# Performance work log

Hardware: AMD Instinct MI355X
Metric: run time of the kernel (lower is better)

## Reference

```python
import jax, jax.numpy as jnp
import numpy as np

NF, NA, H, L, R, B = 100000, 4000, 256, 4, 4, 3
E_FA, E_AF, E_FF, E_AA = 200000, 200000, 400000, 40000
N = NF + NA


def setup_inputs() -> dict:
    key = jax.random.key(0)
    ks = jax.random.split(key, 18)
    inp = {}
    inp["x_flight"] = jax.random.normal(ks[0], (NF, 32), jnp.float32)
    inp["x_airport"] = jax.random.normal(ks[1], (NA, 16), jnp.float32)
    # per-node-type encoder Linears (stored as [in, H] so y = x @ W + b)
    inp["enc_w_flight"] = jax.random.normal(ks[2], (32, H), jnp.float32) / np.sqrt(32.0).astype(np.float32)
    inp["enc_b_flight"] = jnp.zeros((H,), jnp.float32)
    inp["enc_w_airport"] = jax.random.normal(ks[3], (16, H), jnp.float32) / np.sqrt(16.0).astype(np.float32)
    inp["enc_b_airport"] = jnp.zeros((H,), jnp.float32)
    # stacked per-layer RGCNConv params: basis decomposition W_r = sum_b comp[r,b] * basis[b]
    inp["basis"] = jax.random.normal(ks[4], (L, B, H, H), jnp.float32) * 0.02
    inp["comp"] = jax.random.normal(ks[5], (L, R, B), jnp.float32)
    inp["root"] = jax.random.normal(ks[6], (L, H, H), jnp.float32) * 0.02
    inp["conv_bias"] = jnp.zeros((L, H), jnp.float32)
    inp["ln_gamma"] = jnp.ones((L, H), jnp.float32)
    inp["ln_beta"] = jnp.zeros((L, H), jnp.float32)
    inp["ro_w"] = jax.random.normal(ks[7], (H, 1), jnp.float32) / np.sqrt(float(H)).astype(np.float32)
    inp["ro_b"] = jnp.zeros((1,), jnp.float32)
    # hetero edge indices (row 0 = src local id, row 1 = dst local id)
    inp["ei_fa"] = jnp.stack([jax.random.randint(ks[8], (E_FA,), 0, NF),
                               jax.random.randint(ks[9], (E_FA,), 0, NA)]).astype(jnp.int32)
    inp["ei_af"] = jnp.stack([jax.random.randint(ks[10], (E_AF,), 0, NA),
                               jax.random.randint(ks[11], (E_AF,), 0, NF)]).astype(jnp.int32)
    inp["ei_ff"] = jnp.stack([jax.random.randint(ks[12], (E_FF,), 0, NF),
                               jax.random.randint(ks[13], (E_FF,), 0, NF)]).astype(jnp.int32)
    inp["ei_aa"] = jnp.stack([jax.random.randint(ks[14], (E_AA,), 0, NA),
                               jax.random.randint(ks[15], (E_AA,), 0, NA)]).astype(jnp.int32)
    return inp


def _layernorm(x, g, b, eps=1e-5):
    mu = jnp.mean(x, axis=-1, keepdims=True)
    var = jnp.mean(jnp.square(x - mu), axis=-1, keepdims=True)
    return (x - mu) * jax.lax.rsqrt(var + eps) * g + b


def _build_graph(ei_fa, ei_af, ei_ff, ei_aa):
    # node offsets: flight=0, airport=NF (node_types order = ['flight','airport'])
    src = jnp.concatenate([ei_fa[0], ei_af[0] + NF, ei_ff[0], ei_aa[0] + NF])
    dst = jnp.concatenate([ei_fa[1] + NF, ei_af[1], ei_ff[1], ei_aa[1] + NF])
    et = jnp.concatenate([jnp.full((E_FA,), 0, jnp.int32), jnp.full((E_AF,), 1, jnp.int32),
                          jnp.full((E_FF,), 2, jnp.int32), jnp.full((E_AA,), 3, jnp.int32)])
    return src, dst, et


def reference(x_flight, x_airport, enc_w_flight, enc_b_flight, enc_w_airport, enc_b_airport,
              basis, comp, root, conv_bias, ln_gamma, ln_beta, ro_w, ro_b,
              ei_fa, ei_af, ei_ff, ei_aa):
    hf = x_flight @ enc_w_flight + enc_b_flight    # [NF, H]
    ha = x_airport @ enc_w_airport + enc_b_airport  # [NA, H]
    x = jnp.concatenate([hf, ha], axis=0)           # [N, H]

    src, dst, et = _build_graph(ei_fa, ei_af, ei_ff, ei_aa)
    seg = et * N + dst                              # composite (relation, target-node) segment id
    cnt = jax.ops.segment_sum(jnp.ones(src.shape, x.dtype), seg, num_segments=R * N)
    denom = jnp.maximum(cnt.reshape(R, N, 1), 1.0)  # per-relation in-degree (mean aggr)

    for l in range(L):
        x_res = x
        W = jnp.einsum('rb,bio->rio', comp[l], basis[l])                 # [R, H, H]
        agg = jax.ops.segment_sum(x[src], seg, num_segments=R * N)
        agg = agg.reshape(R, N, H) / denom                                # per-relation mean of x_j
        h = jnp.einsum('rnh,rho->no', agg, W) + x @ root[l] + conv_bias[l]
        h = _layernorm(h, ln_gamma[l], ln_beta[l])
        h = jnp.where(h > 0, h, 0.1 * h)                                  # leaky_relu(0.1)
        x = h + x_res                                                     # dropout is identity in eval

    return (x[:NF] @ ro_w + ro_b)[:, 0]             # readout over flight nodes, squeeze(-1)
```

## Files before the change

kernel.cpp:

```cpp
#include <hip/hip_runtime.h>
#include <cstdint>


namespace {

constexpr int kNF = 100000;
constexpr int kNA = 4000;
constexpr int kN  = 104000;
constexpr int kH  = 256;
constexpr int kL  = 4;
constexpr int kB  = 3;
constexpr int kEFA = 200000;
constexpr int kEAF = 200000;
constexpr int kEFF = 400000;
constexpr int kEAA = 40000;
constexpr int kETOT = 840000;
constexpr int kK = 768;
constexpr int kKA = 512;
constexpr int kSEG = 2 * kNA + 2 * kNF;
constexpr int kScanBlocks = (kSEG + 1023) / 1024;

typedef __attribute__((ext_vector_type(8))) short short8v;
typedef __attribute__((ext_vector_type(4))) float float4v;

__device__ __forceinline__ float b2f(unsigned short u) {
  union { unsigned int i; float f; } v;
  v.i = ((unsigned int)u) << 16;
  return v.f;
}
__device__ __forceinline__ unsigned short f2b(float f) {
  union { float f; unsigned int i; } v;
  v.f = f;
  unsigned int x = v.i;
  x += 0x7fffu + ((x >> 16) & 1u);
  return (unsigned short)(x >> 16);
}

__device__ __forceinline__ void gload16(const unsigned short* gsrc,
                                        unsigned short* lds) {
  __builtin_amdgcn_global_load_lds(
      (const __attribute__((address_space(1))) unsigned int*)gsrc,
      (__attribute__((address_space(3))) unsigned int*)lds, 16, 0, 0);
}

__global__ void k_build_encWt(const float* __restrict__ wf,
                              const float* __restrict__ wa,
                              unsigned short* __restrict__ WtF,
                              unsigned short* __restrict__ WtA) {
  const int idx = blockIdx.x * 256 + threadIdx.x;
  if (idx >= 2 * kH * 32) return;
  const int t = idx / (kH * 32);
  const int rem = idx % (kH * 32);
  const int n = rem >> 5;
  const int k = rem & 31;
  if (t == 0) {
    WtF[n * 32 + k] = f2b(wf[k * kH + n]);
  } else {
    WtA[n * 32 + k] = (k < 16) ? f2b(wa[k * kH + n]) : (unsigned short)0;
  }
}

template <int KIN>
__global__ __launch_bounds__(256) void k_enc_mfma(
    const float* __restrict__ xin, const unsigned short* __restrict__ Wt,
    const float* __restrict__ bias, unsigned short* __restrict__ xout, int M,
    int rowoff) {
  __shared__ __align__(16) unsigned short As[64][40];
  const int tid = threadIdx.x;
  const int wave = tid >> 6;
  const int lane = tid & 63;
  const int fr = lane & 15;
  const int fq = lane >> 4;
  const int ncol0 = wave * 64;
  const int brow = blockIdx.x * 64;

  const int row = tid >> 2;
  const int col0 = (tid & 3) * 8;
  float4 f0 = make_float4(0.f, 0.f, 0.f, 0.f);
  float4 f1 = make_float4(0.f, 0.f, 0.f, 0.f);
  if (brow + row < M) {
    if (col0 < KIN) f0 = *(const float4*)&xin[(size_t)(brow + row) * KIN + col0];
    if (col0 + 4 < KIN)
      f1 = *(const float4*)&xin[(size_t)(brow + row) * KIN + col0 + 4];
  }
  uint4 packed;
  packed.x = (unsigned int)f2b(f0.x) | ((unsigned int)f2b(f0.y) << 16);
  packed.y = (unsigned int)f2b(f0.z) | ((unsigned int)f2b(f0.w) << 16);
  packed.z = (unsigned int)f2b(f1.x) | ((unsigned int)f2b(f1.y) << 16);
  packed.w = (unsigned int)f2b(f1.z) | ((unsigned int)f2b(f1.w) << 16);
  *(uint4*)&As[row][col0] = packed;
  __syncthreads();

  short8v bfrag[4];
#pragma unroll
  for (int ni = 0; ni < 4; ++ni)
    bfrag[ni] = *(const short8v*)&Wt[(size_t)(ncol0 + ni * 16 + fr) * 32 + fq * 8];

  float4v acc[4][4];
#pragma unroll
  for (int mi = 0; mi < 4; ++mi) {
    const short8v afrag = *(const short8v*)&As[mi * 16 + fr][fq * 8];
#pragma unroll
    for (int ni = 0; ni < 4; ++ni)
      acc[mi][ni] = __builtin_amdgcn_mfma_f32_16x16x32_bf16(
          afrag, bfrag[ni], (float4v)(0.f), 0, 0, 0);
  }

#pragma unroll
  for (int ni = 0; ni < 4; ++ni) {
    const int col = ncol0 + ni * 16 + fr;
    const float bb = bias[col];
#pragma unroll
    for (int mi = 0; mi < 4; ++mi) {
      const int row0 = brow + mi * 16 + fq * 4;
#pragma unroll
      for (int reg = 0; reg < 4; ++reg) {
        const int r = row0 + reg;
        if (r < M) xout[(size_t)(rowoff + r) * kH + col] = f2b(acc[mi][ni][reg] + bb);
      }
    }
  }
}

__device__ __forceinline__ void edge_decode(int i, const int* ei_fa,
                                            const int* ei_af, const int* ei_ff,
                                            const int* ei_aa, int& src,
                                            int& dstseg) {
  if (i < kEFA) {
    src = ei_fa[i];
    dstseg = 0 + ei_fa[kEFA + i];
  } else if (i < kEFA + kEAF) {
    const int j = i - kEFA;
    src = kNF + ei_af[j];
    dstseg = kNA + ei_af[kEAF + j];
  } else if (i < kEFA + kEAF + kEFF) {
    const int j = i - kEFA - kEAF;
    src = ei_ff[j];
    dstseg = kNA + kNF + ei_ff[kEFF + j];
  } else {
    const int j = i - kEFA - kEAF - kEFF;
    src = kNF + ei_aa[j];
    dstseg = kNA + 2 * kNF + ei_aa[kEAA + j];
  }
}

__global__ void k_count_all(const int* __restrict__ ei_fa,
                            const int* __restrict__ ei_af,
                            const int* __restrict__ ei_ff,
                            const int* __restrict__ ei_aa,
                            int* __restrict__ cnt) {
  const int i = blockIdx.x * 256 + threadIdx.x;
  if (i >= kETOT) return;
  int src, dstseg;
  edge_decode(i, ei_fa, ei_af, ei_ff, ei_aa, src, dstseg);
  atomicAdd(&cnt[dstseg], 1);
}

__global__ void k_scan1(const int* __restrict__ cnt, int* __restrict__ out,
                        int* __restrict__ bsum, float* __restrict__ invdeg) {
  __shared__ int sh[256];
  const int tid = threadIdx.x;
  const int base = blockIdx.x * 1024 + tid * 4;
  int v[4];
#pragma unroll
  for (int j = 0; j < 4; ++j) v[j] = (base + j < kSEG) ? cnt[base + j] : 0;
#pragma unroll
  for (int j = 0; j < 4; ++j)
    if (base + j < kSEG)
      invdeg[base + j] = 1.0f / (float)(v[j] > 0 ? v[j] : 1);
  const int tsum = v[0] + v[1] + v[2] + v[3];
  sh[tid] = tsum;
  __syncthreads();
  for (int o = 1; o < 256; o <<= 1) {
    int t = (tid >= o) ? sh[tid - o] : 0;
    __syncthreads();
    sh[tid] += t;
    __syncthreads();
  }
  const int excl = sh[tid] - tsum;
  int run = excl;
#pragma unroll
  for (int j = 0; j < 4; ++j) {
    if (base + j < kSEG) out[base + j] = run;
    run += v[j];
  }
  if (tid == 255) bsum[blockIdx.x] = sh[255];
}

__global__ void k_scan2(const int* __restrict__ bsum, int* __restrict__ bpre) {
  __shared__ int sh[256];
  const int tid = threadIdx.x;
  const int v = (tid < kScanBlocks) ? bsum[tid] : 0;
  sh[tid] = v;
  __syncthreads();
  for (int o = 1; o < 256; o <<= 1) {
    int t = (tid >= o) ? sh[tid - o] : 0;
    __syncthreads();
    sh[tid] += t;
    __syncthreads();
  }
  if (tid < kScanBlocks) bpre[tid] = sh[tid] - v;
}

__global__ void k_scan3(int* __restrict__ off, int* __restrict__ cursor,
                        const int* __restrict__ bpre) {
  const int i = blockIdx.x * 256 + threadIdx.x;
  if (i < kSEG) {
    const int val = off[i] + bpre[i >> 10];
    off[i] = val;
    cursor[i] = val;
  }
  if (i == 0) off[kSEG] = kETOT;
}

__global__ void k_fill_all(const int* __restrict__ ei_fa,
                           const int* __restrict__ ei_af,
                           const int* __restrict__ ei_ff,
                           const int* __restrict__ ei_aa,
                           int* __restrict__ cursor, int* __restrict__ elist) {
  const int i = blockIdx.x * 256 + threadIdx.x;
  if (i >= kETOT) return;
  int src, dstseg;
  edge_decode(i, ei_fa, ei_af, ei_ff, ei_aa, src, dstseg);
  const int pos = atomicAdd(&cursor[dstseg], 1);
  elist[pos] = src;
}

__global__ void k_build_Bt(const float* __restrict__ comp_l,
                           const float* __restrict__ basis_l,
                           const float* __restrict__ root_l,
                           unsigned short* __restrict__ BtF,
                           unsigned short* __restrict__ BtA) {
  const int idx = blockIdx.x * 256 + threadIdx.x;
  if (idx >= 2 * kK * kH) return;
  const int t = idx / (kK * kH);
  const int rem = idx % (kK * kH);
  const int n = rem / kK;
  const int k = rem % kK;
  const int slot = k >> 8;
  const int wrow = k & 255;
  float val;
  if (slot == 2) {
    val = root_l[wrow * kH + n];
  } else {
    const int r = (t == 0) ? (slot == 0 ? 1 : 2) : (slot == 0 ? 0 : 3);
    const int io = wrow * kH + n;
    val = comp_l[r * kB + 0] * basis_l[0 * kH * kH + io] +
          comp_l[r * kB + 1] * basis_l[1 * kH * kH + io] +
          comp_l[r * kB + 2] * basis_l[2 * kH * kH + io];
  }
  (t == 0 ? BtF : BtA)[(size_t)n * kK + k] = f2b(val);
}

__global__ __launch_bounds__(256) void k_gather2(
    const unsigned short* __restrict__ x, unsigned short* __restrict__ Aagg,
    const int* __restrict__ off, const int* __restrict__ elist,
    const float* __restrict__ invdeg, int segbase0, int segbase1, int c0,
    int nrows) {
  const int half = threadIdx.x >> 5;
  const int lane = threadIdx.x & 31;
  const int d = blockIdx.x * 8 + half;
  const int slot = blockIdx.y;
  if (d >= nrows) return;
  const int s = (slot == 0 ? segbase0 : segbase1) + c0 + d;
  const int lo = off[s], hi = off[s + 1];
  const float iv = invdeg[s];
  float a0 = 0.f, a1 = 0.f, a2 = 0.f, a3 = 0.f;
  float a4 = 0.f, a5 = 0.f, a6 = 0.f, a7 = 0.f;
  const unsigned short* xl = x + lane * 8;
  int e = lo;
  for (; e + 3 < hi; e += 4) {
    const int s0 = elist[e], s1 = elist[e + 1];
    const int s2 = elist[e + 2], s3 = elist[e + 3];
    const uint4 v0 = *(const uint4*)(xl + (size_t)s0 * kH);
    const uint4 v1 = *(const uint4*)(xl + (size_t)s1 * kH);
    const uint4 v2 = *(const uint4*)(xl + (size_t)s2 * kH);
    const uint4 v3 = *(const uint4*)(xl + (size_t)s3 * kH);
    a0 += b2f((unsigned short)v0.x) + b2f((unsigned short)v1.x) +
          b2f((unsigned short)v2.x) + b2f((unsigned short)v3.x);
    a1 += b2f((unsigned short)(v0.x >> 16)) + b2f((unsigned short)(v1.x >> 16)) +
          b2f((unsigned short)(v2.x >> 16)) + b2f((unsigned short)(v3.x >> 16));
    a2 += b2f((unsigned short)v0.y) + b2f((unsigned short)v1.y) +
          b2f((unsigned short)v2.y) + b2f((unsigned short)v3.y);
    a3 += b2f((unsigned short)(v0.y >> 16)) + b2f((unsigned short)(v1.y >> 16)) +
          b2f((unsigned short)(v2.y >> 16)) + b2f((unsigned short)(v3.y >> 16));
    a4 += b2f((unsigned short)v0.z) + b2f((unsigned short)v1.z) +
          b2f((unsigned short)v2.z) + b2f((unsigned short)v3.z);
    a5 += b2f((unsigned short)(v0.z >> 16)) + b2f((unsigned short)(v1.z >> 16)) +
          b2f((unsigned short)(v2.z >> 16)) + b2f((unsigned short)(v3.z >> 16));
    a6 += b2f((unsigned short)v0.w) + b2f((unsigned short)v1.w) +
          b2f((unsigned short)v2.w) + b2f((unsigned short)v3.w);
    a7 += b2f((unsigned short)(v0.w >> 16)) + b2f((unsigned short)(v1.w >> 16)) +
          b2f((unsigned short)(v2.w >> 16)) + b2f((unsigned short)(v3.w >> 16));
  }
  for (; e < hi; ++e) {
    const int s0 = elist[e];
    const uint4 v0 = *(const uint4*)(xl + (size_t)s0 * kH);
    a0 += b2f((unsigned short)v0.x);
    a1 += b2f((unsigned short)(v0.x >> 16));
    a2 += b2f((unsigned short)v0.y);
    a3 += b2f((unsigned short)(v0.y >> 16));
    a4 += b2f((unsigned short)v0.z);
    a5 += b2f((unsigned short)(v0.z >> 16));
    a6 += b2f((unsigned short)v0.w);
    a7 += b2f((unsigned short)(v0.w >> 16));
  }
  uint4 o;
  o.x = (unsigned int)f2b(a0 * iv) | ((unsigned int)f2b(a1 * iv) << 16);
  o.y = (unsigned int)f2b(a2 * iv) | ((unsigned int)f2b(a3 * iv) << 16);
  o.z = (unsigned int)f2b(a4 * iv) | ((unsigned int)f2b(a5 * iv) << 16);
  o.w = (unsigned int)f2b(a6 * iv) | ((unsigned int)f2b(a7 * iv) << 16);
  *(uint4*)&Aagg[(size_t)d * kKA + slot * kH + lane * 8] = o;
}

__global__ __launch_bounds__(256) void k_gemm_fused(
    const unsigned short* __restrict__ Aagg,
    const unsigned short* __restrict__ xcur, unsigned short* __restrict__ xnxt,
    const unsigned short* __restrict__ Bt, const float* __restrict__ bias,
    const float* __restrict__ gamma, const float* __restrict__ beta, int M,
    int grow0) {
  __shared__ __align__(16) unsigned short As[3][64][32];
  __shared__ __align__(16) unsigned short Bs[3][256][32];
  __shared__ float redS[4][64];
  __shared__ float redQ[4][64];
  __shared__ float stat[64][2];

  const int tid = threadIdx.x;
  const int wave = tid >> 6;
  const int lane = tid & 63;
  const int fr = lane & 15;
  const int fq = lane >> 4;
  const int ncol0 = wave * 64;
  const int brow = blockIdx.x * 64;

  const int srow = lane >> 2;
  const int sg = (lane & 3) ^ (srow & 3);
  const int arow = wave * 16 + srow;
  const unsigned short* Asrc_agg = Aagg + (size_t)(brow + arow) * kKA + sg * 8;
  const unsigned short* Asrc_x =
      xcur + (size_t)(grow0 + brow + arow) * kH + sg * 8;
  const unsigned short* Bsrc = Bt + (size_t)(wave * 64 + srow) * kK + sg * 8;

#define STAGE(buf, t)                                                         \
  do {                                                                        \
    const int kb_ = (t) * 32;                                                 \
    gload16((kb_ < kKA) ? (Asrc_agg + kb_) : (Asrc_x + (kb_ - kKA)),          \
            &As[buf][wave * 16][0]);                                          \
    _Pragma("unroll") for (int j_ = 0; j_ < 4; ++j_)                          \
        gload16(Bsrc + (size_t)(j_ * 16) * kK + kb_,                          \
                &Bs[buf][wave * 64 + j_ * 16][0]);                            \
  } while (0)

  float4v acc[4][4];
#pragma unroll
  for (int mi = 0; mi < 4; ++mi)
#pragma unroll
    for (int ni = 0; ni < 4; ++ni) acc[mi][ni] = (float4v)(0.f);

  const int rg = (fr & 3);

  STAGE(0, 0);
  STAGE(1, 1);
  asm volatile("s_waitcnt vmcnt(5)" ::: "memory");
  asm volatile("s_barrier" ::: "memory");

  for (int t = 0; t < 24; ++t) {
    const int cur = t % 3;
    short8v afrag[4], bfrag[4];
#pragma unroll
    for (int mi = 0; mi < 4; ++mi)
      afrag[mi] = *(const short8v*)&As[cur][mi * 16 + fr][(fq ^ rg) * 8];
#pragma unroll
    for (int ni = 0; ni < 4; ++ni)
      bfrag[ni] =
          *(const short8v*)&Bs[cur][ncol0 + ni * 16 + fr][(fq ^ rg) * 8];
    asm volatile("s_waitcnt lgkmcnt(0)" ::: "memory");
    if (t < 22) STAGE((t + 2) % 3, t + 2);
#pragma unroll
    for (int mi = 0; mi < 4; ++mi)
#pragma unroll
      for (int ni = 0; ni < 4; ++ni)
        acc[mi][ni] = __builtin_amdgcn_mfma_f32_16x16x32_bf16(
            afrag[mi], bfrag[ni], acc[mi][ni], 0, 0, 0);
    if (t < 22) {
      asm volatile("s_waitcnt vmcnt(5)" ::: "memory");
    } else {
      asm volatile("s_waitcnt vmcnt(0)" ::: "memory");
    }
    asm volatile("s_barrier" ::: "memory");
  }
#undef STAGE

  float bb[4], gam[4], bet[4];
#pragma unroll
  for (int ni = 0; ni < 4; ++ni) {
    const int col = ncol0 + ni * 16 + fr;
    bb[ni] = bias[col];
    gam[ni] = gamma[col];
    bet[ni] = beta[col];
  }
#pragma unroll
  for (int mi = 0; mi < 4; ++mi)
#pragma unroll
    for (int ni = 0; ni < 4; ++ni)
#pragma unroll
      for (int reg = 0; reg < 4; ++reg) acc[mi][ni][reg] += bb[ni];

#pragma unroll
  for (int mi = 0; mi < 4; ++mi) {
#pragma unroll
    for (int reg = 0; reg < 4; ++reg) {
      float s = 0.f, q = 0.f;
#pragma unroll
      for (int ni = 0; ni < 4; ++ni) {
        const float v = acc[mi][ni][reg];
        s += v;
        q += v * v;
      }
#pragma unroll
      for (int o = 1; o < 16; o <<= 1) {
        s += __shfl_xor(s, o);
        q += __shfl_xor(q, o);
      }
      if (fr == 0) {
        const int rl = mi * 16 + fq * 4 + reg;
        redS[wave][rl] = s;
        redQ[wave][rl] = q;
      }
    }
  }
  __syncthreads();
  if (tid < 64) {
    const float s = redS[0][tid] + redS[1][tid] + redS[2][tid] + redS[3][tid];
    const float q = redQ[0][tid] + redQ[1][tid] + redQ[2][tid] + redQ[3][tid];
    const float mu = s * (1.f / kH);
    const float var = q * (1.f / kH) - mu * mu;
    stat[tid][0] = mu;
    stat[tid][1] = rsqrtf(var + 1e-5f);
  }
  __syncthreads();

#pragma unroll
  for (int mi = 0; mi < 4; ++mi) {
#pragma unroll
    for (int reg = 0; reg < 4; ++reg) {
      const int rl = mi * 16 + fq * 4 + reg;
      const int r = brow + rl;
      if (r >= M) continue;
      const float mu = stat[rl][0];
      const float rs = stat[rl][1];
      const size_t gr = (size_t)(grow0 + r) * kH;
#pragma unroll
      for (int ni = 0; ni < 4; ++ni) {
        const int col = ncol0 + ni * 16 + fr;
        float t = (acc[mi][ni][reg] - mu) * rs * gam[ni] + bet[ni];
        t = t > 0.f ? t : 0.1f * t;
        const float xo = b2f(xcur[gr + col]);
        xnxt[gr + col] = f2b(xo + t);
      }
    }
  }
}

__global__ __launch_bounds__(256) void k_readout(
    const unsigned short* __restrict__ x, const float* __restrict__ w,
    const float* __restrict__ b, float* __restrict__ out) {
  const int wave = threadIdx.x >> 6;
  const int lane = threadIdx.x & 63;
  const int row = blockIdx.x * 4 + wave;
  if (row >= kNF) return;
  const ushort4 v = *(const ushort4*)&x[(size_t)row * kH + (lane << 2)];
  const float4 wv = *(const float4*)&w[lane << 2];
  float s = b2f(v.x) * wv.x + b2f(v.y) * wv.y + b2f(v.z) * wv.z +
            b2f(v.w) * wv.w;
#pragma unroll
  for (int o = 1; o < 64; o <<= 1) s += __shfl_xor(s, o);
  if (lane == 0) out[row] = s + b[0];
}

}

extern "C" void kernel_launch(void* const* d_in, const int* in_sizes, int n_in,
                              void* d_out, int out_size, void* d_ws,
                              size_t ws_size, hipStream_t stream) {
  const float* x_flight = (const float*)d_in[0];
  const float* x_airport = (const float*)d_in[1];
  const float* enc_w_f = (const float*)d_in[2];
  const float* enc_b_f = (const float*)d_in[3];
  const float* enc_w_a = (const float*)d_in[4];
  const float* enc_b_a = (const float*)d_in[5];
  const float* basis = (const float*)d_in[6];
  const float* comp = (const float*)d_in[7];
  const float* root = (const float*)d_in[8];
  const float* conv_bias = (const float*)d_in[9];
  const float* ln_gamma = (const float*)d_in[10];
  const float* ln_beta = (const float*)d_in[11];
  const float* ro_w = (const float*)d_in[12];
  const float* ro_b = (const float*)d_in[13];
  const int* ei_fa = (const int*)d_in[14];
  const int* ei_af = (const int*)d_in[15];
  const int* ei_ff = (const int*)d_in[16];
  const int* ei_aa = (const int*)d_in[17];
  float* out = (float*)d_out;

  char* base = (char*)d_ws;
  size_t off_b = 0;
  auto carve = [&](size_t bytes) -> char* {
    char* p = base + off_b;
    off_b += (bytes + 255) & ~(size_t)255;
    return p;
  };
  unsigned short* xbuf = (unsigned short*)carve((size_t)kN * kH * 2);
  unsigned short* hbuf = (unsigned short*)carve((size_t)kN * kH * 2);
  unsigned short* BtF = (unsigned short*)carve((size_t)kK * kH * 2);
  unsigned short* BtA = (unsigned short*)carve((size_t)kK * kH * 2);
  unsigned short* WtF = (unsigned short*)carve((size_t)kH * 32 * 2);
  unsigned short* WtA = (unsigned short*)carve((size_t)kH * 32 * 2);
  int* cnt = (int*)carve((size_t)kSEG * 4);
  int* offs = (int*)carve((size_t)(kSEG + 1) * 4);
  int* cursor = (int*)carve((size_t)kSEG * 4);
  int* elist = (int*)carve((size_t)kETOT * 4);
  int* bsum = (int*)carve((size_t)kScanBlocks * 4);
  int* bpre = (int*)carve((size_t)kScanBlocks * 4);
  float* invdeg = (float*)carve((size_t)kSEG * 4);
  size_t rem = (ws_size > off_b + 4096) ? (ws_size - off_b - 4096) : 0;
  int CH = (int)(rem / ((size_t)kKA * 2)) - 64;
  if (CH > 102400) CH = 102400;
  CH &= ~63;
  if (CH < 64) CH = 64;
  unsigned short* Achunk = (unsigned short*)carve((size_t)(CH + 64) * kKA * 2);

  k_build_encWt<<<(2 * kH * 32 + 255) / 256, 256, 0, stream>>>(enc_w_f, enc_w_a,
                                                               WtF, WtA);
  k_enc_mfma<32><<<(kNF + 63) / 64, 256, 0, stream>>>(x_flight, WtF, enc_b_f,
                                                      xbuf, kNF, 0);
  k_enc_mfma<16><<<(kNA + 63) / 64, 256, 0, stream>>>(x_airport, WtA, enc_b_a,
                                                      xbuf, kNA, kNF);

  hipMemsetAsync(cnt, 0, (size_t)kSEG * 4, stream);
  const int b0 = 0, b1 = kNA, b2 = kNA + kNF, b3 = kNA + 2 * kNF;
  k_count_all<<<(kETOT + 255) / 256, 256, 0, stream>>>(ei_fa, ei_af, ei_ff,
                                                       ei_aa, cnt);
  k_scan1<<<kScanBlocks, 256, 0, stream>>>(cnt, offs, bsum, invdeg);
  k_scan2<<<1, 256, 0, stream>>>(bsum, bpre);
  k_scan3<<<(kSEG + 255) / 256, 256, 0, stream>>>(offs, cursor, bpre);
  k_fill_all<<<(kETOT + 255) / 256, 256, 0, stream>>>(ei_fa, ei_af, ei_ff,
                                                      ei_aa, cursor, elist);

  unsigned short* bufs[2] = {xbuf, hbuf};
  int curb = 0;
  for (int l = 0; l < kL; ++l) {
    const float* comp_l = comp + (size_t)l * 4 * kB;
    const float* basis_l = basis + (size_t)l * kB * kH * kH;
    const float* root_l = root + (size_t)l * kH * kH;
    const float* bias_l = conv_bias + (size_t)l * kH;
    const float* gamma_l = ln_gamma + (size_t)l * kH;
    const float* beta_l = ln_beta + (size_t)l * kH;
    const unsigned short* xc = bufs[curb];
    unsigned short* xn = bufs[curb ^ 1];

    k_build_Bt<<<(2 * kK * kH + 255) / 256, 256, 0, stream>>>(comp_l, basis_l,
                                                              root_l, BtF, BtA);

    for (int c0 = 0; c0 < kNF; c0 += CH) {
      const int rows = (kNF - c0 < CH) ? (kNF - c0) : CH;
      dim3 gg((rows + 7) / 8, 2);
      k_gather2<<<gg, 256, 0, stream>>>(xc, Achunk, offs, elist, invdeg, b1,
                                        b2, c0, rows);
      dim3 g((rows + 63) / 64);
      k_gemm_fused<<<g, 256, 0, stream>>>(Achunk, xc, xn, BtF, bias_l, gamma_l,
                                          beta_l, rows, c0);
    }
    for (int c0 = 0; c0 < kNA; c0 += CH) {
      const int rows = (kNA - c0 < CH) ? (kNA - c0) : CH;
      dim3 gg((rows + 7) / 8, 2);
      k_gather2<<<gg, 256, 0, stream>>>(xc, Achunk, offs, elist, invdeg, b0,
                                        b3, c0, rows);
      dim3 g((rows + 63) / 64);
      k_gemm_fused<<<g, 256, 0, stream>>>(Achunk, xc, xn, BtA, bias_l, gamma_l,
                                          beta_l, rows, kNF + c0);
    }
    curb ^= 1;
  }

  k_readout<<<(kNF + 3) / 4, 256, 0, stream>>>(bufs[curb], ro_w, ro_b, out);
}
```

Before: 1.068 ms.

## Split fused GEMM across eight waves with 32-column tiles per wave

The fused GEMM+LayerNorm kernel now launches 512 threads per block, and each of the eight waves computes a 64x32 output slice instead of 64x64. Only the first four waves stage A tiles, and each wave waits only on its own count of outstanding async loads. The LDS swizzle is changed to XOR with a wider row-derived pattern. The aim is more waves per CU and fewer accumulator registers per wave, at the cost of more barrier participants and an eight-way cross-wave LayerNorm reduction.

```diff
diff --git a/kernel.cpp b/kernel.cpp
--- a/kernel.cpp
+++ b/kernel.cpp
@@ -41,6 +41,10 @@
   __builtin_amdgcn_global_load_lds(
       (const __attribute__((address_space(1))) unsigned int*)gsrc,
       (__attribute__((address_space(3))) unsigned int*)lds, 16, 0, 0);
+}
+
+__device__ __forceinline__ int swz16(int r) {
+  return (r & 3) ^ ((r >> 2) & 3);
 }
 
 __global__ void k_build_encWt(const float* __restrict__ wf,
@@ -313,7 +317,7 @@
   *(uint4*)&Aagg[(size_t)d * kKA + slot * kH + lane * 8] = o;
 }
 
-__global__ __launch_bounds__(256) void k_gemm_fused(
+__global__ __launch_bounds__(512) void k_gemm_fused(
     const unsigned short* __restrict__ Aagg,
     const unsigned short* __restrict__ xcur, unsigned short* __restrict__ xnxt,
     const unsigned short* __restrict__ Bt, const float* __restrict__ bias,
@@ -321,8 +325,8 @@
     int grow0) {
   __shared__ __align__(16) unsigned short As[3][64][32];
   __shared__ __align__(16) unsigned short Bs[3][256][32];
-  __shared__ float redS[4][64];
-  __shared__ float redQ[4][64];
+  __shared__ float redS[8][64];
+  __shared__ float redQ[8][64];
   __shared__ float stat[64][2];
 
   const int tid = threadIdx.x;
@@ -330,70 +334,78 @@
   const int lane = tid & 63;
   const int fr = lane & 15;
   const int fq = lane >> 4;
-  const int ncol0 = wave * 64;
+  const int ncol0 = wave * 32;
   const int brow = blockIdx.x * 64;
 
   const int srow = lane >> 2;
-  const int sg = (lane & 3) ^ (srow & 3);
-  const int arow = wave * 16 + srow;
-  const unsigned short* Asrc_agg = Aagg + (size_t)(brow + arow) * kKA + sg * 8;
+  const int sg = (lane & 3) ^ swz16(srow);
+  const unsigned short* Asrc_agg =
+      Aagg + (size_t)(brow + wave * 16 + srow) * kKA + sg * 8;
   const unsigned short* Asrc_x =
-      xcur + (size_t)(grow0 + brow + arow) * kH + sg * 8;
-  const unsigned short* Bsrc = Bt + (size_t)(wave * 64 + srow) * kK + sg * 8;
+      xcur + (size_t)(grow0 + brow + wave * 16 + srow) * kH + sg * 8;
+  const unsigned short* Bsrc = Bt + (size_t)(wave * 32 + srow) * kK + sg * 8;
 
 #define STAGE(buf, t)                                                         \
   do {                                                                        \
     const int kb_ = (t) * 32;                                                 \
-    gload16((kb_ < kKA) ? (Asrc_agg + kb_) : (Asrc_x + (kb_ - kKA)),          \
-            &As[buf][wave * 16][0]);                                          \
-    _Pragma("unroll") for (int j_ = 0; j_ < 4; ++j_)                          \
-        gload16(Bsrc + (size_t)(j_ * 16) * kK + kb_,                          \
-                &Bs[buf][wave * 64 + j_ * 16][0]);                            \
+    if (wave < 4)                                                             \
+      gload16((kb_ < kKA) ? (Asrc_agg + kb_) : (Asrc_x + (kb_ - kKA)),        \
+              &As[buf][wave * 16][0]);                                        \
+    gload16(Bsrc + kb_, &Bs[buf][wave * 32][0]);                              \
+    gload16(Bsrc + (size_t)16 * kK + kb_, &Bs[buf][wave * 32 + 16][0]);       \
   } while (0)
-
-  float4v acc[4][4];
+#define WAIT_OWN()                                                            \
+  do {                                                                        \
+    if (wave < 4)                                                             \
+      asm volatile("s_waitcnt vmcnt(3)" ::: "memory");                        \
+    else                                                                      \
+      asm volatile("s_waitcnt vmcnt(2)" ::: "memory");                        \
+  } while (0)
+
+  float4v acc[4][2];
 #pragma unroll
   for (int mi = 0; mi < 4; ++mi)
 #pragma unroll
-    for (int ni = 0; ni < 4; ++ni) acc[mi][ni] = (float4v)(0.f);
-
-  const int rg = (fr & 3);
+    for (int ni = 0; ni < 2; ++ni) acc[mi][ni] = (float4v)(0.f);
+
+  const int rg = swz16(fr);
 
   STAGE(0, 0);
   STAGE(1, 1);
-  asm volatile("s_waitcnt vmcnt(5)" ::: "memory");
+  WAIT_OWN();
   asm volatile("s_barrier" ::: "memory");
 
   for (int t = 0; t < 24; ++t) {
     const int cur = t % 3;
-    short8v afrag[4], bfrag[4];
+    short8v afrag[4], bfrag[2];
 #pragma unroll
     for (int mi = 0; mi < 4; ++mi)
-      afrag[mi] = *(const short8v*)&As[cur][mi * 16 + fr][(fq ^ rg) * 8];
-#pragma unroll
-    for (int ni = 0; ni < 4; ++ni)
+      afrag[mi] = *(const short8v*)&As[cur][mi * 16 + fr][((fq ^ rg) & 3) * 8];
+#pragma unroll
+    for (int ni = 0; ni < 2; ++ni)
       bfrag[ni] =
-          *(const short8v*)&Bs[cur][ncol0 + ni * 16 + fr][(fq ^ rg) * 8];
+          *(const short8v*)&Bs[cur][ncol0 + ni * 16 + fr][((fq ^ rg) & 3) * 8];
     asm volatile("s_waitcnt lgkmcnt(0)" ::: "memory");
     if (t < 22) STAGE((t + 2) % 3, t + 2);
 #pragma unroll
     for (int mi = 0; mi < 4; ++mi)
 #pragma unroll
-      for (int ni = 0; ni < 4; ++ni)
+      for (int ni = 0; ni < 2; ++ni)
         acc[mi][ni] = __builtin_amdgcn_mfma_f32_16x16x32_bf16(
             afrag[mi], bfrag[ni], acc[mi][ni], 0, 0, 0);
     if (t < 22) {
-      asm volatile("s_waitcnt vmcnt(5)" ::: "memory");
+      WAIT_OWN();
     } else {
       asm volatile("s_waitcnt vmcnt(0)" ::: "memory");
     }
     asm volatile("s_barrier" ::: "memory");
   }
 #undef STAGE
-
-  float bb[4], gam[4], bet[4];
-#pragma unroll
-  for (int ni = 0; ni < 4; ++ni) {
+#undef WAIT_OWN
+
+  float bb[2], gam[2], bet[2];
+#pragma unroll
+  for (int ni = 0; ni < 2; ++ni) {
     const int col = ncol0 + ni * 16 + fr;
     bb[ni] = bias[col];
     gam[ni] = gamma[col];
@@ -402,7 +414,7 @@
 #pragma unroll
   for (int mi = 0; mi < 4; ++mi)
 #pragma unroll
-    for (int ni = 0; ni < 4; ++ni)
+    for (int ni = 0; ni < 2; ++ni)
 #pragma unroll
       for (int reg = 0; reg < 4; ++reg) acc[mi][ni][reg] += bb[ni];
 
@@ -412,7 +424,7 @@
     for (int reg = 0; reg < 4; ++reg) {
       float s = 0.f, q = 0.f;
 #pragma unroll
-      for (int ni = 0; ni < 4; ++ni) {
+      for (int ni = 0; ni < 2; ++ni) {
         const float v = acc[mi][ni][reg];
         s += v;
         q += v * v;
@@ -431,8 +443,12 @@
   }
   __syncthreads();
   if (tid < 64) {
-    const float s = redS[0][tid] + redS[1][tid] + redS[2][tid] + redS[3][tid];
-    const float q = redQ[0][tid] + redQ[1][tid] + redQ[2][tid] + redQ[3][tid];
+    float s = 0.f, q = 0.f;
+#pragma unroll
+    for (int w = 0; w < 8; ++w) {
+      s += redS[w][tid];
+      q += redQ[w][tid];
+    }
     const float mu = s * (1.f / kH);
     const float var = q * (1.f / kH) - mu * mu;
     stat[tid][0] = mu;
@@ -451,7 +467,7 @@
       const float rs = stat[rl][1];
       const size_t gr = (size_t)(grow0 + r) * kH;
 #pragma unroll
-      for (int ni = 0; ni < 4; ++ni) {
+      for (int ni = 0; ni < 2; ++ni) {
         const int col = ncol0 + ni * 16 + fr;
         float t = (acc[mi][ni][reg] - mu) * rs * gam[ni] + bet[ni];
         t = t > 0.f ? t : 0.1f * t;
@@ -568,7 +584,7 @@
       k_gather2<<<gg, 256, 0, stream>>>(xc, Achunk, offs, elist, invdeg, b1,
                                         b2, c0, rows);
       dim3 g((rows + 63) / 64);
-      k_gemm_fused<<<g, 256, 0, stream>>>(Achunk, xc, xn, BtF, bias_l, gamma_l,
+      k_gemm_fused<<<g, 512, 0, stream>>>(Achunk, xc, xn, BtF, bias_l, gamma_l,
                                           beta_l, rows, c0);
     }
     for (int c0 = 0; c0 < kNA; c0 += CH) {
@@ -577,7 +593,7 @@
       k_gather2<<<gg, 256, 0, stream>>>(xc, Achunk, offs, elist, invdeg, b0,
                                         b3, c0, rows);
       dim3 g((rows + 63) / 64);
-      k_gemm_fused<<<g, 256, 0, stream>>>(Achunk, xc, xn, BtA, bias_l, gamma_l,
+      k_gemm_fused<<<g, 512, 0, stream>>>(Achunk, xc, xn, BtA, bias_l, gamma_l,
                                           beta_l, rows, kNF + c0);
     }
     curb ^= 1;
```

After: 1.061 ms. Within noise of the previous version (-0.7%).
